# Kernel optimization log

Hardware: AMD Instinct MI355X
Metric: run time of the kernel (lower is better)

The kernel has to match this reference:

```python
import jax, jax.numpy as jnp
import numpy as np

K = 20
EPS = 1e-5
SLOPE = 0.2


def knn_idx(x, k):
    # x: (B, N, C) -> indices of k nearest neighbors (B, N, k), includes self
    xx = jnp.sum(x * x, axis=-1)                       # (B, N)
    inner = jnp.einsum('bnc,bmc->bnm', x, x)           # (B, N, N)
    neg_d = 2.0 * inner - xx[:, :, None] - xx[:, None, :]  # -||xi-xj||^2
    return jax.lax.top_k(neg_d, k)[1]                  # (B, N, k)


def get_graph_feature(x, k):
    # x: (B, N, C) -> (B, N, k, 2C) = [nbr - center, center]
    idx = knn_idx(x, k)
    nbr = jax.vmap(lambda xb, ib: xb[ib])(x, idx)      # (B, N, k, C) gather
    center = x[:, :, None, :]
    return jnp.concatenate([nbr - center, jnp.broadcast_to(center, nbr.shape)], axis=-1)


def bn(h, axes, g, b):
    # training-mode batch norm over `axes`, channels on last axis
    m = jnp.mean(h, axes, keepdims=True)
    v = jnp.var(h, axes, keepdims=True)
    return (h - m) * jax.lax.rsqrt(v + EPS) * g + b


def leaky(h):
    return jnp.where(h > 0, h, SLOPE * h)


def edge_conv(x, W, g, b):
    # x: (B, N, C) -> (B, N, C_out); 1x1 conv + BN + LeakyReLU + max over k
    f = get_graph_feature(x, K)                        # (B, N, k, 2C)
    h = jnp.einsum('bnkc,oc->bnko', f, W)
    h = leaky(bn(h, (0, 1, 2), g, b))
    return jnp.max(h, axis=2)


def setup_inputs() -> dict:
    key = jax.random.key(0)
    ks = jax.random.split(key, 6)
    B, N = 2, 4096
    x = jax.random.normal(ks[0], (B, 3, N), jnp.float32)

    def w(k_, o, i):
        return jax.random.normal(k_, (o, i), jnp.float32) * (1.0 / np.sqrt(i))

    ones = lambda c: jnp.ones((c,), jnp.float32)
    zeros = lambda c: jnp.zeros((c,), jnp.float32)
    return dict(
        x=x,
        W1=w(ks[1], 64, 6),   g1=ones(64),   b1=zeros(64),
        W2=w(ks[2], 64, 128), g2=ones(64),   b2=zeros(64),
        W3=w(ks[3], 128, 128), g3=ones(128), b3=zeros(128),
        W4=w(ks[4], 256, 256), g4=ones(256), b4=zeros(256),
        W5=w(ks[5], 1024, 512), g5=ones(1024), b5=zeros(1024),
    )


def reference(x, W1, g1, b1, W2, g2, b2, W3, g3, b3, W4, g4, b4, W5, g5, b5):
    xb = x.transpose(0, 2, 1)                          # (B, N, 3)
    x1 = edge_conv(xb, W1, g1, b1)                     # (B, N, 64)
    x2 = edge_conv(x1, W2, g2, b2)                     # (B, N, 64)
    x3 = edge_conv(x2, W3, g3, b3)                     # (B, N, 128)
    x4 = edge_conv(x3, W4, g4, b4)                     # (B, N, 256)
    cat = jnp.concatenate([x1, x2, x3, x4], axis=-1)   # (B, N, 512)
    h = jnp.einsum('bnc,oc->bno', cat, W5)             # (B, N, 1024)
    h = leaky(bn(h, (0, 1), g5, b5))
    return h.transpose(0, 2, 1)                        # (B, 1024, N)
```

## Files before the change

### kernel.cpp

```cpp
#include <hip/hip_runtime.h>
#include <cmath>

#define KNN 20
#define NPTS 4096
#define BATCH 2
#define SLOPE 0.2f
#define BNEPS 1e-5
#define GTK 16
#define MAXCAND 256

typedef unsigned short u16;
typedef __attribute__((ext_vector_type(8))) short bf16x8;
typedef __attribute__((ext_vector_type(4))) float f32x4;
typedef _Float16 h8 __attribute__((ext_vector_type(8)));
typedef _Float16 h4 __attribute__((ext_vector_type(4)));

static __device__ __host__ inline int imin(int a, int b) { return a < b ? a : b; }

__global__ void xtrans_kernel(const float* __restrict__ x, float* __restrict__ xb) {
  int i = blockIdx.x * 256 + threadIdx.x;
  if (i < BATCH * 3 * NPTS) {
    int b = i / (3 * NPTS);
    int r = i - b * 3 * NPTS;
    int c = r / NPTS;
    int n = r - c * NPTS;
    xb[((size_t)b * NPTS + n) * 3 + c] = x[i];
  }
}

__global__ void uprep_kernel(const float* __restrict__ W, float* __restrict__ U, int O, int C) {
  int i = blockIdx.x * 256 + threadIdx.x;
  if (i < C * O) {
    int j = i / O, o = i - j * O;
    float w1 = W[(size_t)o * 2 * C + j];
    float w2 = W[(size_t)o * 2 * C + C + j];
    U[(size_t)j * 2 * O + o] = w1;
    U[(size_t)j * 2 * O + O + o] = w2 - w1;
  }
}

__global__ void xx_kernel(const float* __restrict__ X, int stride, int C, float* __restrict__ xx) {
  int i = blockIdx.x * 256 + threadIdx.x;
  if (i < BATCH * NPTS) {
    const float* r = X + (size_t)i * stride;
    double s = 0.0;
    for (int c = 0; c < C; ++c) s += (double)r[c] * (double)r[c];
    xx[i] = (float)s;
  }
}

__global__ void tobf16_kernel(const float* __restrict__ src, u16* __restrict__ dst, int n4) {
  int i = blockIdx.x * 256 + threadIdx.x;
  if (i < n4) {
    float4 v = *(const float4*)&src[(size_t)i * 4];
    unsigned o[4];
#pragma unroll
    for (int j = 0; j < 4; ++j) {
      unsigned x = __float_as_uint(((const float*)&v)[j]);
      unsigned rr = x + 0x7fff + ((x >> 16) & 1);
      o[j] = rr >> 16;
    }
    uint2 pk;
    pk.x = o[0] | (o[1] << 16);
    pk.y = o[2] | (o[3] << 16);
    *(uint2*)&dst[(size_t)i * 4] = pk;
  }
}

template <bool BT, bool DIST>
__global__ __launch_bounds__(256) void gemm128(const float* __restrict__ A, int lda,
                                               const float* __restrict__ B, int ldb,
                                               void* __restrict__ Cout, int ldc, int K,
                                               const float* __restrict__ xxA,
                                               const float* __restrict__ xxB) {
  __shared__ __align__(16) float sA[GTK][144];
  __shared__ __align__(16) float sB[GTK][144];
  int t = threadIdx.x;
  int tx = t & 15, ty = t >> 4;
  int row0 = blockIdx.y * 128, col0 = blockIdx.x * 128;
  float acc[8][8] = {};

  for (int k0 = 0; k0 < K; k0 += GTK) {
    bool fast = (k0 + GTK <= K);
    if (fast) {
#pragma unroll
      for (int it = 0; it < 2; ++it) {
        int i = t + it * 256;
        int r = i >> 2, q = i & 3;
        const float4 av = *(const float4*)&A[(size_t)(row0 + r) * lda + k0 + q * 4];
        int pr = r + ((r >> 5) << 2);
        sA[q * 4 + 0][pr] = av.x;
        sA[q * 4 + 1][pr] = av.y;
        sA[q * 4 + 2][pr] = av.z;
        sA[q * 4 + 3][pr] = av.w;
      }
    } else {
#pragma unroll
      for (int it = 0; it < 2; ++it) {
        int i = t + it * 256;
        int r = i >> 2, q = i & 3;
        int pr = r + ((r >> 5) << 2);
#pragma unroll
        for (int j = 0; j < 4; ++j) {
          int k = q * 4 + j;
          sA[k][pr] = (k0 + k < K) ? A[(size_t)(row0 + r) * lda + k0 + k] : 0.f;
        }
      }
    }
    if (BT) {
      if (fast) {
#pragma unroll
        for (int it = 0; it < 2; ++it) {
          int i = t + it * 256;
          int r = i >> 2, q = i & 3;
          const float4 bv = *(const float4*)&B[(size_t)(col0 + r) * ldb + k0 + q * 4];
          int pr = r + ((r >> 5) << 2);
          sB[q * 4 + 0][pr] = bv.x;
          sB[q * 4 + 1][pr] = bv.y;
          sB[q * 4 + 2][pr] = bv.z;
          sB[q * 4 + 3][pr] = bv.w;
        }
      } else {
#pragma unroll
        for (int it = 0; it < 2; ++it) {
          int i = t + it * 256;
          int r = i >> 2, q = i & 3;
          int pr = r + ((r >> 5) << 2);
#pragma unroll
          for (int j = 0; j < 4; ++j) {
            int k = q * 4 + j;
            sB[k][pr] = (k0 + k < K) ? B[(size_t)(col0 + r) * ldb + k0 + k] : 0.f;
          }
        }
      }
    } else {
#pragma unroll
      for (int it = 0; it < 2; ++it) {
        int i = t + it * 256;
        int k = i >> 5, nq = (i & 31) * 4;
        int pc = nq + ((nq >> 5) << 2);
        float4 bv = make_float4(0.f, 0.f, 0.f, 0.f);
        if (k0 + k < K) bv = *(const float4*)&B[(size_t)(k0 + k) * ldb + col0 + nq];
        *(float4*)&sB[k][pc] = bv;
      }
    }
    __syncthreads();
    int prA = ty * 8 + ((ty >> 2) << 2);
    int prB = tx * 8 + ((tx >> 2) << 2);
#pragma unroll
    for (int kk = 0; kk < GTK; ++kk) {
      float a[8], b[8];
      *(float4*)&a[0] = *(const float4*)&sA[kk][prA];
      *(float4*)&a[4] = *(const float4*)&sA[kk][prA + 4];
      *(float4*)&b[0] = *(const float4*)&sB[kk][prB];
      *(float4*)&b[4] = *(const float4*)&sB[kk][prB + 4];
#pragma unroll
      for (int i = 0; i < 8; ++i)
#pragma unroll
        for (int j = 0; j < 8; ++j) acc[i][j] += a[i] * b[j];
    }
    __syncthreads();
  }

  if (DIST) {
    _Float16* Ch = (_Float16*)Cout;
#pragma unroll
    for (int i = 0; i < 8; ++i) {
      int gr = row0 + ty * 8 + i;
      float xa = xxA[gr];
      h8 o;
#pragma unroll
      for (int j = 0; j < 8; ++j) {
        int gc = col0 + tx * 8 + j;
        o[j] = (_Float16)(2.f * acc[i][j] - xa - xxB[gc]);
      }
      *(h8*)&Ch[(size_t)gr * ldc + col0 + tx * 8] = o;
    }
  } else {
    float* Cf = (float*)Cout;
#pragma unroll
    for (int i = 0; i < 8; ++i) {
      int gr = row0 + ty * 8 + i;
#pragma unroll
      for (int jq = 0; jq < 2; ++jq) {
        float4 o;
#pragma unroll
        for (int j = 0; j < 4; ++j) ((float*)&o)[j] = acc[i][jq * 4 + j];
        *(float4*)&Cf[(size_t)gr * ldc + col0 + tx * 8 + jq * 4] = o;
      }
    }
  }
}

__global__ __launch_bounds__(256) void gemm_dist_sym_kernel(const float* __restrict__ X, int lda,
                                                            const float* __restrict__ xx,
                                                            _Float16* __restrict__ dist, int K,
                                                            size_t dstride) {
  __shared__ __align__(16) float sA[GTK][144];
  __shared__ __align__(16) float sB[GTK][144];
  int t = threadIdx.x;
  int tx = t & 15, ty = t >> 4;
  const float* Xb = X + (size_t)blockIdx.y * NPTS * lda;
  const float* xxv = xx + (size_t)blockIdx.y * NPTS;
  _Float16* db = dist + (size_t)blockIdx.y * dstride;
  int l = blockIdx.x;
  int bi = (int)((sqrtf(8.f * (float)l + 1.f) - 1.f) * 0.5f);
  while ((bi + 1) * (bi + 2) / 2 <= l) ++bi;
  while (bi * (bi + 1) / 2 > l) --bi;
  int bj = l - bi * (bi + 1) / 2;
  int row0 = bi * 128, col0 = bj * 128;
  float acc[8][8] = {};

  for (int k0 = 0; k0 < K; k0 += GTK) {
#pragma unroll
    for (int it = 0; it < 2; ++it) {
      int i = t + it * 256;
      int r = i >> 2, q = i & 3;
      const float4 av = *(const float4*)&Xb[(size_t)(row0 + r) * lda + k0 + q * 4];
      const float4 bv = *(const float4*)&Xb[(size_t)(col0 + r) * lda + k0 + q * 4];
      int pr = r + ((r >> 5) << 2);
      sA[q * 4 + 0][pr] = av.x;
      sA[q * 4 + 1][pr] = av.y;
      sA[q * 4 + 2][pr] = av.z;
      sA[q * 4 + 3][pr] = av.w;
      sB[q * 4 + 0][pr] = bv.x;
      sB[q * 4 + 1][pr] = bv.y;
      sB[q * 4 + 2][pr] = bv.z;
      sB[q * 4 + 3][pr] = bv.w;
    }
    __syncthreads();
    int prA = ty * 8 + ((ty >> 2) << 2);
    int prB = tx * 8 + ((tx >> 2) << 2);
#pragma unroll
    for (int kk = 0; kk < GTK; ++kk) {
      float a[8], b[8];
      *(float4*)&a[0] = *(const float4*)&sA[kk][prA];
      *(float4*)&a[4] = *(const float4*)&sA[kk][prA + 4];
      *(float4*)&b[0] = *(const float4*)&sB[kk][prB];
      *(float4*)&b[4] = *(const float4*)&sB[kk][prB + 4];
#pragma unroll
      for (int i = 0; i < 8; ++i)
#pragma unroll
        for (int j = 0; j < 8; ++j) acc[i][j] += a[i] * b[j];
    }
    __syncthreads();
  }

  {
    float xa[8], xb_[8];
#pragma unroll
    for (int i = 0; i < 8; ++i) xa[i] = xxv[row0 + ty * 8 + i];
#pragma unroll
    for (int j = 0; j < 8; ++j) xb_[j] = xxv[col0 + tx * 8 + j];
#pragma unroll
    for (int i = 0; i < 8; ++i)
#pragma unroll
      for (int j = 0; j < 8; ++j) acc[i][j] = 2.f * acc[i][j] - xa[i] - xb_[j];
  }
#pragma unroll
  for (int i = 0; i < 8; ++i) {
    h8 o;
#pragma unroll
    for (int j = 0; j < 8; ++j) o[j] = (_Float16)acc[i][j];
    *(h8*)&db[(size_t)(row0 + ty * 8 + i) * NPTS + col0 + tx * 8] = o;
  }
  if (bi != bj) {
#pragma unroll
    for (int j = 0; j < 8; ++j) {
      h8 o;
#pragma unroll
      for (int i = 0; i < 8; ++i) o[i] = (_Float16)acc[i][j];
      *(h8*)&db[(size_t)(col0 + tx * 8 + j) * NPTS + row0 + ty * 8] = o;
    }
  }
}

__global__ __launch_bounds__(256) void fc_mfma_kernel(const u16* __restrict__ A,
                                                      const u16* __restrict__ B,
                                                      float* __restrict__ C) {
  __shared__ u16 sA[128][56];
  __shared__ u16 sB[128][56];
  int t = threadIdx.x;
  int lane = t & 63, wave = t >> 6;
  int row0 = blockIdx.y * 128, col0 = blockIdx.x * 128;
  int wr = (wave >> 1) * 64, wc = (wave & 1) * 64;
  int m = lane & 15, q = lane >> 4;
  f32x4 acc[4][4];
#pragma unroll
  for (int i = 0; i < 4; ++i)
#pragma unroll
    for (int j = 0; j < 4; ++j) acc[i][j] = (f32x4){0.f, 0.f, 0.f, 0.f};
  for (int k0 = 0; k0 < 512; k0 += 32) {
#pragma unroll
    for (int it = 0; it < 2; ++it) {
      int i = t + it * 256;
      int r = i >> 2, ch = (i & 3) * 8;
      *(uint4*)&sA[r][ch] = *(const uint4*)&A[(size_t)(row0 + r) * 512 + k0 + ch];
      *(uint4*)&sB[r][ch] = *(const uint4*)&B[(size_t)(col0 + r) * 512 + k0 + ch];
    }
    __syncthreads();
    bf16x8 af[4], bf[4];
#pragma unroll
    for (int i = 0; i < 4; ++i) af[i] = *(const bf16x8*)&sA[wr + i * 16 + m][q * 8];
#pragma unroll
    for (int j = 0; j < 4; ++j) bf[j] = *(const bf16x8*)&sB[wc + j * 16 + m][q * 8];
#pragma unroll
    for (int i = 0; i < 4; ++i)
#pragma unroll
      for (int j = 0; j < 4; ++j)
        acc[i][j] = __builtin_amdgcn_mfma_f32_16x16x32_bf16(af[i], bf[j], acc[i][j], 0, 0, 0);
    __syncthreads();
  }
#pragma unroll
  for (int i = 0; i < 4; ++i)
#pragma unroll
    for (int j = 0; j < 4; ++j)
#pragma unroll
      for (int reg = 0; reg < 4; ++reg)
        C[(size_t)(row0 + wr + i * 16 + q * 4 + reg) * 1024 + col0 + wc + j * 16 + m] =
            acc[i][j][reg];
}

__device__ inline bool comp_less(double v, int i, double ov, int oi) {
  return (v < ov) || (v == ov && i > oi);
}

__global__ __launch_bounds__(256) void topk_fast_kernel(const _Float16* __restrict__ dist,
                                                        size_t dstride,
                                                        const float* __restrict__ Xb,
                                                        size_t xstride, int lda, int C,
                                                        int* __restrict__ idxout, size_t istride,
                                                        int n0, int rows) {
  __shared__ int scand[4][MAXCAND];
  int wave = threadIdx.x >> 6, lane = threadIdx.x & 63;
  int row = blockIdx.x * 4 + wave;
  if (row >= rows) return;
  const _Float16* distb = dist + (size_t)blockIdx.y * dstride;
  const float* Xbb = Xb + (size_t)blockIdx.y * xstride;
  int* idxb = idxout + (size_t)blockIdx.y * istride;
  const _Float16* d = distb + (size_t)row * NPTS;
  float v[16][4];
  float lmax = -__builtin_inff();
#pragma unroll
  for (int s = 0; s < 16; ++s) {
    h4 hv = *(const h4*)&d[s * 256 + lane * 4];
#pragma unroll
    for (int c = 0; c < 4; ++c) {
      v[s][c] = (float)hv[c];
      lmax = fmaxf(lmax, v[s][c]);
    }
  }

  float sv = lmax;
  for (int k = 2; k <= 64; k <<= 1) {
    for (int j = k >> 1; j > 0; j >>= 1) {
      float ov = __shfl_xor(sv, j);
      bool up = ((lane & k) == 0);
      bool lower = ((lane & j) == 0);
      bool mineLess = sv < ov;
      bool keepMine = (up == lower) ? mineLess : !mineLess;
      sv = keepMine ? sv : ov;
    }
  }
  float T = __shfl(sv, 44);

  int myCnt = 0;
#pragma unroll
  for (int s = 0; s < 16; ++s)
#pragma unroll
    for (int c = 0; c < 4; ++c) myCnt += (v[s][c] >= T) ? 1 : 0;
  int ofs = myCnt;
  for (int dlt = 1; dlt < 64; dlt <<= 1) {
    int o = __shfl_up(ofs, dlt);
    if (lane >= dlt) ofs += o;
  }
  int total = __shfl(ofs, 63);
  ofs -= myCnt;
  int w = ofs;
#pragma unroll
  for (int s = 0; s < 16; ++s)
#pragma unroll
    for (int c = 0; c < 4; ++c) {
      if (v[s][c] >= T) {
        if (w < MAXCAND) scand[wave][w] = s * 256 + lane * 4 + c;
        ++w;
      }
    }
  int cnt = imin(total, MAXCAND);
  int gn = n0 + row;
  const float* crow = Xbb + (size_t)gn * lda;
  int nch = (cnt + 63) >> 6;

  double runV = -__builtin_inf();
  int runI = 0x7fffffff;
  for (int ch = 0; ch < nch; ++ch) {
    int slot = ch * 64 + lane;
    int m = (slot < cnt) ? scand[wave][slot] : -1;
    double val = -__builtin_inf();
    int vi = 0x7fffffff;
    if (m >= 0) {
      const float* mrow = Xbb + (size_t)m * lda;
      double dd = 0.0;
      for (int c = 0; c < C; c += 4) {
        float4 a = *(const float4*)&crow[c];
        float4 b = *(const float4*)&mrow[c];
#pragma unroll
        for (int qq = 0; qq < 4; ++qq) {
          double df = (double)((const float*)&a)[qq] - (double)((const float*)&b)[qq];
          dd = fma(df, df, dd);
        }
      }
      val = -dd;
      vi = m;
    }
    for (int k = 2; k <= 64; k <<= 1) {
      for (int j = k >> 1; j > 0; j >>= 1) {
        double ov = __shfl_xor(val, j);
        int oi = __shfl_xor(vi, j);
        bool up = ((lane & k) == 0);
        bool lower = ((lane & j) == 0);
        bool mineLess = comp_less(val, vi, ov, oi);
        bool keepMine = (up == lower) ? mineLess : !mineLess;
        if (!keepMine) { val = ov; vi = oi; }
      }
    }
    if (ch == 0) {
      runV = val;
      runI = vi;
    } else {
      double rv = __shfl(val, 63 - lane);
      int ri = __shfl(vi, 63 - lane);
      if (comp_less(runV, runI, rv, ri)) { runV = rv; runI = ri; }
      for (int j = 32; j > 0; j >>= 1) {
        double ov = __shfl_xor(runV, j);
        int oi = __shfl_xor(runI, j);
        bool lower = ((lane & j) == 0);
        bool mineLess = comp_less(runV, runI, ov, oi);
        bool keepMine = lower ? mineLess : !mineLess;
        if (!keepMine) { runV = ov; runI = oi; }
      }
    }
  }
  if (lane >= 44) idxb[(size_t)gn * KNN + (63 - lane)] = runI;
}

__global__ __launch_bounds__(256) void dist3_topk_kernel(const float* __restrict__ Xb,
                                                         int* __restrict__ idxout) {
  __shared__ float xs[NPTS], ys[NPTS], zs[NPTS];
  __shared__ int scand[4][MAXCAND];
  int t = threadIdx.x;
  const float* Xbb = Xb + (size_t)blockIdx.y * NPTS * 3;
  for (int i = t; i < NPTS * 3; i += 256) {
    int n = i / 3, c = i - n * 3;
    float v = Xbb[i];
    if (c == 0) xs[n] = v;
    else if (c == 1) ys[n] = v;
    else zs[n] = v;
  }
  __syncthreads();
  int wave = t >> 6, lane = t & 63;
  int row = blockIdx.x * 4 + wave;
  float cx = xs[row], cy = ys[row], cz = zs[row];
  float v[16][4];
  float lmax = -__builtin_inff();
#pragma unroll
  for (int s = 0; s < 16; ++s)
#pragma unroll
    for (int c = 0; c < 4; ++c) {
      int m = s * 256 + c * 64 + lane;
      float dx = cx - xs[m], dy = cy - ys[m], dz = cz - zs[m];
      float dv = -(dx * dx + dy * dy + dz * dz);
      v[s][c] = dv;
      lmax = fmaxf(lmax, dv);
    }

  float sv = lmax;
  for (int k = 2; k <= 64; k <<= 1) {
    for (int j = k >> 1; j > 0; j >>= 1) {
      float ov = __shfl_xor(sv, j);
      bool up = ((lane & k) == 0);
      bool lower = ((lane & j) == 0);
      bool mineLess = sv < ov;
      bool keepMine = (up == lower) ? mineLess : !mineLess;
      sv = keepMine ? sv : ov;
    }
  }
  float T = __shfl(sv, 44);

  int myCnt = 0;
#pragma unroll
  for (int s = 0; s < 16; ++s)
#pragma unroll
    for (int c = 0; c < 4; ++c) myCnt += (v[s][c] >= T) ? 1 : 0;
  int ofs = myCnt;
  for (int dlt = 1; dlt < 64; dlt <<= 1) {
    int o = __shfl_up(ofs, dlt);
    if (lane >= dlt) ofs += o;
  }
  int total = __shfl(ofs, 63);
  ofs -= myCnt;
  int w = ofs;
#pragma unroll
  for (int s = 0; s < 16; ++s)
#pragma unroll
    for (int c = 0; c < 4; ++c) {
      if (v[s][c] >= T) {
        if (w < MAXCAND) scand[wave][w] = s * 256 + c * 64 + lane;
        ++w;
      }
    }
  int cnt = imin(total, MAXCAND);
  int nch = (cnt + 63) >> 6;

  double runV = -__builtin_inf();
  int runI = 0x7fffffff;
  for (int ch = 0; ch < nch; ++ch) {
    int slot = ch * 64 + lane;
    int m = (slot < cnt) ? scand[wave][slot] : -1;
    double val = -__builtin_inf();
    int vi = 0x7fffffff;
    if (m >= 0) {
      double dx = (double)cx - (double)xs[m];
      double dy = (double)cy - (double)ys[m];
      double dz = (double)cz - (double)zs[m];
      val = -(dx * dx + dy * dy + dz * dz);
      vi = m;
    }
    for (int k = 2; k <= 64; k <<= 1) {
      for (int j = k >> 1; j > 0; j >>= 1) {
        double ov = __shfl_xor(val, j);
        int oi = __shfl_xor(vi, j);
        bool up = ((lane & k) == 0);
        bool lower = ((lane & j) == 0);
        bool mineLess = comp_less(val, vi, ov, oi);
        bool keepMine = (up == lower) ? mineLess : !mineLess;
        if (!keepMine) { val = ov; vi = oi; }
      }
    }
    if (ch == 0) {
      runV = val;
      runI = vi;
    } else {
      double rv = __shfl(val, 63 - lane);
      int ri = __shfl(vi, 63 - lane);
      if (comp_less(runV, runI, rv, ri)) { runV = rv; runI = ri; }
      for (int j = 32; j > 0; j >>= 1) {
        double ov = __shfl_xor(runV, j);
        int oi = __shfl_xor(runI, j);
        bool lower = ((lane & j) == 0);
        bool mineLess = comp_less(runV, runI, ov, oi);
        bool keepMine = lower ? mineLess : !mineLess;
        if (!keepMine) { runV = ov; runI = oi; }
      }
    }
  }
  if (lane >= 44)
    idxout[((size_t)blockIdx.y * NPTS + row) * KNN + (63 - lane)] = runI;
}

template <int NO>
__global__ __launch_bounds__(256) void gathermax_kernel(const float* __restrict__ PQ,
                                                        const int* __restrict__ idx,
                                                        float* __restrict__ hmax, int O,
                                                        double* __restrict__ pbuf) {
  __shared__ double sh1[4][256];
  __shared__ double sh2[4][256];
  int t = threadIdx.x;
  int wave = t >> 6, lane = t & 63;
  int pt = blockIdx.x * 4 + wave;
  int b = pt >> 12;
  int O2 = 2 * O;
  int iv = idx[(size_t)pt * KNN + (lane % KNN)];
  const float* Qp = PQ + (size_t)pt * O2 + O + lane * NO;
  float q[NO], mx[NO];
  double s1[NO], s2[NO];
#pragma unroll
  for (int c = 0; c < NO; ++c) {
    q[c] = Qp[c];
    mx[c] = -__builtin_inff();
    s1[c] = 0.0;
    s2[c] = 0.0;
  }
#pragma unroll
  for (int k = 0; k < KNN; ++k) {
    int m = __shfl(iv, k);
    const float* Pp = PQ + ((size_t)(b << 12) + m) * O2 + lane * NO;
    float p[NO];
#pragma unroll
    for (int c = 0; c < NO; ++c) p[c] = Pp[c];
#pragma unroll
    for (int c = 0; c < NO; ++c) {
      float h = p[c] + q[c];
      mx[c] = fmaxf(mx[c], h);
      double hd = (double)h;
      s1[c] += hd;
      s2[c] += hd * hd;
    }
  }
  float* Hp = hmax + (size_t)pt * O + lane * NO;
#pragma unroll
  for (int c = 0; c < NO; ++c) {
    Hp[c] = mx[c];
    sh1[wave][lane * NO + c] = s1[c];
    sh2[wave][lane * NO + c] = s2[c];
  }
  __syncthreads();
  if (t < O) {
    double a = 0.0, bb = 0.0;
#pragma unroll
    for (int w = 0; w < 4; ++w) {
      a += sh1[w][t];
      bb += sh2[w][t];
    }
    pbuf[(size_t)blockIdx.x * O2 + t] = a;
    pbuf[(size_t)blockIdx.x * O2 + O + t] = bb;
  }
}

__global__ __launch_bounds__(256) void bn_reduce_finalize(const double* __restrict__ pbuf,
                                                          int nblk, int O,
                                                          const float* __restrict__ g,
                                                          const float* __restrict__ bb,
                                                          double invcount,
                                                          float* __restrict__ s_out,
                                                          float* __restrict__ t_out) {
  __shared__ double sh1[256];
  __shared__ double sh2[256];
  int o = blockIdx.x;
  int t = threadIdx.x;
  double s1 = 0.0, s2 = 0.0;
  for (int blk = t; blk < nblk; blk += 256) {
    s1 += pbuf[(size_t)blk * 2 * O + o];
    s2 += pbuf[(size_t)blk * 2 * O + O + o];
  }
  sh1[t] = s1;
  sh2[t] = s2;
  __syncthreads();
  for (int s = 128; s > 0; s >>= 1) {
    if (t < s) {
      sh1[t] += sh1[t + s];
      sh2[t] += sh2[t + s];
    }
    __syncthreads();
  }
  if (t == 0) {
    double mean = sh1[0] * invcount;
    double var = sh2[0] * invcount - mean * mean;
    double s = (double)g[o] / sqrt(var + BNEPS);
    s_out[o] = (float)s;
    t_out[o] = (float)((double)bb[o] - mean * s);
  }
}

__global__ void apply_kernel(const float* __restrict__ hmax, const float* __restrict__ s,
                             const float* __restrict__ tt, float* __restrict__ feat,
                             u16* __restrict__ featbf, int colOff, int logO, int total) {
  int i = blockIdx.x * 256 + threadIdx.x;
  if (i >= total) return;
  int O = 1 << logO;
  int o = i & (O - 1);
  int pp = i >> logO;
  float v = hmax[i] * s[o] + tt[o];
  float r = v > 0.f ? v : SLOPE * v;
  size_t di = (size_t)pp * 512 + colOff + o;
  feat[di] = r;
  unsigned xbits = __float_as_uint(r);
  unsigned rr = xbits + 0x7fff + ((xbits >> 16) & 1);
  featbf[di] = (u16)(rr >> 16);
}

__global__ void colstats_kernel(const float* __restrict__ H, double* __restrict__ pbuf) {
  int o = blockIdx.x * 256 + threadIdx.x;
  int rb = blockIdx.y;
  int r0 = rb * 128;
  double s1 = 0.0, s2 = 0.0;
  for (int r = 0; r < 128; ++r) {
    double v = (double)H[(size_t)(r0 + r) * 1024 + o];
    s1 += v;
    s2 += v * v;
  }
  pbuf[(size_t)rb * 2048 + o] = s1;
  pbuf[(size_t)rb * 2048 + 1024 + o] = s2;
}

__global__ void out_kernel(const float* __restrict__ h5, const float* __restrict__ s,
                           const float* __restrict__ tt, float* __restrict__ out) {
  __shared__ float tile[32][33];
  int b = blockIdx.z;
  int n0 = blockIdx.x * 32, o0 = blockIdx.y * 32;
  int t = threadIdx.x;
  for (int e = t; e < 1024; e += 256) {
    int rn = e >> 5, co = e & 31;
    int o = o0 + co;
    float v = h5[((size_t)b * NPTS + n0 + rn) * 1024 + o] * s[o] + tt[o];
    tile[rn][co] = v > 0.f ? v : SLOPE * v;
  }
  __syncthreads();
  for (int e = t; e < 1024; e += 256) {
    int ro = e >> 5, cn = e & 31;
    out[((size_t)b * 1024 + o0 + ro) * NPTS + n0 + cn] = tile[cn][ro];
  }
}

extern "C" void kernel_launch(void* const* d_in, const int* in_sizes, int n_in,
                              void* d_out, int out_size, void* d_ws, size_t ws_size,
                              hipStream_t stream) {
  const float* x = (const float*)d_in[0];
  const float* Wm[5] = {(const float*)d_in[1], (const float*)d_in[4], (const float*)d_in[7],
                        (const float*)d_in[10], (const float*)d_in[13]};
  const float* gv[5] = {(const float*)d_in[2], (const float*)d_in[5], (const float*)d_in[8],
                        (const float*)d_in[11], (const float*)d_in[14]};
  const float* bvv[5] = {(const float*)d_in[3], (const float*)d_in[6], (const float*)d_in[9],
                         (const float*)d_in[12], (const float*)d_in[15]};
  float* out = (float*)d_out;

  char* wsb = (char*)d_ws;
  size_t off = 0;
  auto alloc = [&](size_t bytes) -> char* {
    off = (off + 255) & ~(size_t)255;
    char* p = wsb + off;
    off += bytes;
    return p;
  };
  float* xb = (float*)alloc((size_t)BATCH * NPTS * 3 * 4);
  float* xxb = (float*)alloc((size_t)BATCH * NPTS * 4);
  int* idxb = (int*)alloc((size_t)BATCH * NPTS * KNN * 4);
  float* feat = (float*)alloc((size_t)BATCH * NPTS * 512 * 4);
  float* hmax = (float*)alloc((size_t)BATCH * NPTS * 256 * 4);
  float* h5 = (float*)alloc((size_t)BATCH * NPTS * 1024 * 4);
  float* PQ = h5;
  float* U1 = (float*)alloc(3 * 128 * 4);
  float* U2 = (float*)alloc(64 * 128 * 4);
  float* U3 = (float*)alloc(64 * 256 * 4);
  float* U4 = (float*)alloc(128 * 512 * 4);
  u16* featbf = (u16*)alloc((size_t)BATCH * NPTS * 512 * 2);
  u16* w5bf = (u16*)alloc((size_t)1024 * 512 * 2);
  double* pbuf = (double*)alloc((size_t)2048 * 512 * 8);
  float* stv = (float*)alloc(3072 * 4);
  off = (off + 255) & ~(size_t)255;
  size_t avail = (ws_size > off) ? (ws_size - off) : 0;
  size_t slab = (size_t)NPTS * NPTS * 2;
  int nbfit = (int)imin((int)(avail / slab), BATCH);
  size_t rmax = avail / ((size_t)NPTS * 2);
  int R;
  if (rmax >= NPTS) R = NPTS;
  else {
    R = (int)(rmax & ~(size_t)127);
    if (R < 128) R = 128;
  }
  _Float16* distbuf = (_Float16*)(wsb + off);

  float* sv[5] = {stv + 0, stv + 128, stv + 256, stv + 512, stv + 1024};
  float* tv[5] = {stv + 64, stv + 192, stv + 384, stv + 768, stv + 2048};
  float* Us[4] = {U1, U2, U3, U4};
  const int Cs[4] = {3, 64, 64, 128};
  const int Osz[4] = {64, 64, 128, 256};
  const int ntile = (NPTS / 128) * (NPTS / 128 + 1) / 2;

  xtrans_kernel<<<(BATCH * 3 * NPTS + 255) / 256, 256, 0, stream>>>(x, xb);
  for (int l = 0; l < 4; ++l)
    uprep_kernel<<<(Cs[l] * Osz[l] + 255) / 256, 256, 0, stream>>>(Wm[l], Us[l], Osz[l], Cs[l]);
  tobf16_kernel<<<(1024 * 512 / 4 + 255) / 256, 256, 0, stream>>>(Wm[4], w5bf, 1024 * 512 / 4);

  auto knn = [&](const float* Xbase, int lda, int C) {
    xx_kernel<<<(BATCH * NPTS + 255) / 256, 256, 0, stream>>>(Xbase, lda, C, xxb);
    size_t selems = (size_t)NPTS * NPTS;
    if (nbfit >= BATCH) {
      gemm_dist_sym_kernel<<<dim3(ntile, BATCH), 256, 0, stream>>>(Xbase, lda, xxb, distbuf, C,
                                                                   selems);
      topk_fast_kernel<<<dim3(NPTS / 4, BATCH), 256, 0, stream>>>(
          distbuf, selems, Xbase, (size_t)NPTS * lda, lda, C, idxb, (size_t)NPTS * KNN, 0, NPTS);
    } else if (nbfit >= 1) {
      for (int b = 0; b < BATCH; ++b) {
        const float* Xb = Xbase + (size_t)b * NPTS * lda;
        gemm_dist_sym_kernel<<<dim3(ntile, 1), 256, 0, stream>>>(Xb, lda, xxb + (size_t)b * NPTS,
                                                                 distbuf, C, 0);
        topk_fast_kernel<<<dim3(NPTS / 4, 1), 256, 0, stream>>>(
            distbuf, 0, Xb, 0, lda, C, idxb + (size_t)b * NPTS * KNN, 0, 0, NPTS);
      }
    } else {
      for (int b = 0; b < BATCH; ++b) {
        const float* Xb = Xbase + (size_t)b * NPTS * lda;
        for (int n0 = 0; n0 < NPTS; n0 += R) {
          int rows = imin(R, NPTS - n0);
          gemm128<true, true><<<dim3(NPTS / 128, rows / 128), 256, 0, stream>>>(
              Xb + (size_t)n0 * lda, lda, Xb, lda, (void*)distbuf, NPTS, C,
              xxb + (size_t)b * NPTS + n0, xxb + (size_t)b * NPTS);
          topk_fast_kernel<<<dim3(rows / 4, 1), 256, 0, stream>>>(
              distbuf, 0, Xb, 0, lda, C, idxb + (size_t)b * NPTS * KNN, 0, n0, rows);
        }
      }
    }
  };

  auto edge = [&](int li, const float* Xbase, int lda, int C, int O, int colOff) {
    if (li == 0) {
      dist3_topk_kernel<<<dim3(NPTS / 4, BATCH), 256, 0, stream>>>(Xbase, idxb);
    } else {
      knn(Xbase, lda, C);
    }
    int O2 = 2 * O;
    gemm128<false, false><<<dim3(O2 / 128, BATCH * NPTS / 128), 256, 0, stream>>>(
        Xbase, lda, Us[li], O2, (void*)PQ, O2, C, nullptr, nullptr);
    int nblk = BATCH * NPTS / 4;
    if (O == 64)
      gathermax_kernel<1><<<nblk, 256, 0, stream>>>(PQ, idxb, hmax, O, pbuf);
    else if (O == 128)
      gathermax_kernel<2><<<nblk, 256, 0, stream>>>(PQ, idxb, hmax, O, pbuf);
    else
      gathermax_kernel<4><<<nblk, 256, 0, stream>>>(PQ, idxb, hmax, O, pbuf);
    bn_reduce_finalize<<<O, 256, 0, stream>>>(pbuf, nblk, O, gv[li], bvv[li],
                                              1.0 / ((double)BATCH * NPTS * KNN), sv[li], tv[li]);
    int logO = (O == 64) ? 6 : (O == 128) ? 7 : 8;
    int total = BATCH * NPTS * O;
    apply_kernel<<<(total + 255) / 256, 256, 0, stream>>>(hmax, sv[li], tv[li], feat, featbf,
                                                          colOff, logO, total);
  };

  edge(0, xb, 3, 3, 64, 0);
  edge(1, feat, 512, 64, 64, 64);
  edge(2, feat + 64, 512, 64, 128, 128);
  edge(3, feat + 128, 512, 128, 256, 256);

  fc_mfma_kernel<<<dim3(1024 / 128, BATCH * NPTS / 128), 256, 0, stream>>>(featbf, w5bf, h5);
  colstats_kernel<<<dim3(4, 64), 256, 0, stream>>>(h5, pbuf);
  bn_reduce_finalize<<<1024, 256, 0, stream>>>(pbuf, 64, 1024, gv[4], bvv[4],
                                               1.0 / ((double)BATCH * NPTS), sv[4], tv[4]);
  out_kernel<<<dim3(NPTS / 32, 1024 / 32, BATCH), 256, 0, stream>>>(h5, sv[4], tv[4], out);
}
```

Before: 643.1 us.

## Compute kNN distance tiles with split-bf16 MFMA instead of FP32 FMA

Replaces the FP32 scalar-FMA symmetric distance GEMM with a matrix-core kernel. Point features are first split into high and low bf16 halves by a new kernel. The inner products are then accumulated with three bf16 MFMA products (hi·hi, hi·lo, lo·hi) to keep near-FP32 accuracy. The fp16 output tile is staged through shared memory so both the direct and the transposed stores are coalesced. This costs an extra conversion pass, a split buffer, and a small precision difference that could change neighbour ordering on near-ties.

```diff
diff --git a/kernel.cpp b/kernel.cpp
--- a/kernel.cpp
+++ b/kernel.cpp
@@ -16,6 +16,12 @@
 typedef _Float16 h4 __attribute__((ext_vector_type(4)));
 
 static __device__ __host__ inline int imin(int a, int b) { return a < b ? a : b; }
+
+__device__ inline u16 f2bf(float v) {
+  unsigned x = __float_as_uint(v);
+  unsigned rr = x + 0x7fff + ((x >> 16) & 1);
+  return (u16)(rr >> 16);
+}
 
 __global__ void xtrans_kernel(const float* __restrict__ x, float* __restrict__ xb) {
   int i = blockIdx.x * 256 + threadIdx.x;
@@ -55,16 +61,39 @@
     float4 v = *(const float4*)&src[(size_t)i * 4];
     unsigned o[4];
 #pragma unroll
-    for (int j = 0; j < 4; ++j) {
-      unsigned x = __float_as_uint(((const float*)&v)[j]);
-      unsigned rr = x + 0x7fff + ((x >> 16) & 1);
-      o[j] = rr >> 16;
-    }
+    for (int j = 0; j < 4; ++j) o[j] = f2bf(((const float*)&v)[j]);
     uint2 pk;
     pk.x = o[0] | (o[1] << 16);
     pk.y = o[2] | (o[3] << 16);
     *(uint2*)&dst[(size_t)i * 4] = pk;
   }
+}
+
+__global__ void tosplit_kernel(const float* __restrict__ X, int lda, int C,
+                               u16* __restrict__ hi, u16* __restrict__ lo, int ngroups) {
+  int g = blockIdx.x * 256 + threadIdx.x;
+  if (g >= ngroups) return;
+  int perRow = C >> 2;
+  int r = g / perRow;
+  int cq = (g - r * perRow) * 4;
+  float4 v = *(const float4*)&X[(size_t)r * lda + cq];
+  unsigned ho[4], lo_[4];
+#pragma unroll
+  for (int j = 0; j < 4; ++j) {
+    float f = ((const float*)&v)[j];
+    u16 h = f2bf(f);
+    float hv = __uint_as_float(((unsigned)h) << 16);
+    ho[j] = h;
+    lo_[j] = f2bf(f - hv);
+  }
+  uint2 ph, pl;
+  ph.x = ho[0] | (ho[1] << 16);
+  ph.y = ho[2] | (ho[3] << 16);
+  pl.x = lo_[0] | (lo_[1] << 16);
+  pl.y = lo_[2] | (lo_[3] << 16);
+  size_t di = (size_t)r * C + cq;
+  *(uint2*)&hi[di] = ph;
+  *(uint2*)&lo[di] = pl;
 }
 
 template <bool BT, bool DIST>
@@ -192,15 +221,16 @@
   }
 }
 
-__global__ __launch_bounds__(256) void gemm_dist_sym_kernel(const float* __restrict__ X, int lda,
+__global__ __launch_bounds__(256) void dist_sym_mfma_kernel(const u16* __restrict__ Xhi,
+                                                            const u16* __restrict__ Xlo, int K,
                                                             const float* __restrict__ xx,
-                                                            _Float16* __restrict__ dist, int K,
+                                                            _Float16* __restrict__ dist,
                                                             size_t dstride) {
-  __shared__ __align__(16) float sA[GTK][144];
-  __shared__ __align__(16) float sB[GTK][144];
+  __shared__ __align__(16) u16 smem[20544];
   int t = threadIdx.x;
-  int tx = t & 15, ty = t >> 4;
-  const float* Xb = X + (size_t)blockIdx.y * NPTS * lda;
+  int lane = t & 63, wave = t >> 6;
+  const u16* xh = Xhi + (size_t)blockIdx.y * NPTS * K;
+  const u16* xl = Xlo + (size_t)blockIdx.y * NPTS * K;
   const float* xxv = xx + (size_t)blockIdx.y * NPTS;
   _Float16* db = dist + (size_t)blockIdx.y * dstride;
   int l = blockIdx.x;
@@ -209,68 +239,76 @@
   while (bi * (bi + 1) / 2 > l) --bi;
   int bj = l - bi * (bi + 1) / 2;
   int row0 = bi * 128, col0 = bj * 128;
-  float acc[8][8] = {};
-
-  for (int k0 = 0; k0 < K; k0 += GTK) {
-#pragma unroll
-    for (int it = 0; it < 2; ++it) {
-      int i = t + it * 256;
-      int r = i >> 2, q = i & 3;
-      const float4 av = *(const float4*)&Xb[(size_t)(row0 + r) * lda + k0 + q * 4];
-      const float4 bv = *(const float4*)&Xb[(size_t)(col0 + r) * lda + k0 + q * 4];
-      int pr = r + ((r >> 5) << 2);
-      sA[q * 4 + 0][pr] = av.x;
-      sA[q * 4 + 1][pr] = av.y;
-      sA[q * 4 + 2][pr] = av.z;
-      sA[q * 4 + 3][pr] = av.w;
-      sB[q * 4 + 0][pr] = bv.x;
-      sB[q * 4 + 1][pr] = bv.y;
-      sB[q * 4 + 2][pr] = bv.z;
-      sB[q * 4 + 3][pr] = bv.w;
+  int wr = (wave >> 1) * 64, wc = (wave & 1) * 64;
+  int m = lane & 15, q = lane >> 4;
+  f32x4 acc[4][4];
+#pragma unroll
+  for (int i = 0; i < 4; ++i)
+#pragma unroll
+    for (int j = 0; j < 4; ++j) acc[i][j] = (f32x4){0.f, 0.f, 0.f, 0.f};
+
+  for (int k0 = 0; k0 < K; k0 += 32) {
+#pragma unroll
+    for (int it = 0; it < 8; ++it) {
+      int e = t + it * 256;
+      int a = e >> 9, idx = e & 511;
+      int r = idx >> 2, qq = idx & 3;
+      const u16* src = (a == 0 || a == 2) ? xh : xl;
+      int base = (a < 2) ? row0 : col0;
+      *(uint4*)&smem[a * 5120 + r * 40 + qq * 8] =
+          *(const uint4*)&src[(size_t)(base + r) * K + k0 + qq * 8];
     }
     __syncthreads();
-    int prA = ty * 8 + ((ty >> 2) << 2);
-    int prB = tx * 8 + ((tx >> 2) << 2);
-#pragma unroll
-    for (int kk = 0; kk < GTK; ++kk) {
-      float a[8], b[8];
-      *(float4*)&a[0] = *(const float4*)&sA[kk][prA];
-      *(float4*)&a[4] = *(const float4*)&sA[kk][prA + 4];
-      *(float4*)&b[0] = *(const float4*)&sB[kk][prB];
-      *(float4*)&b[4] = *(const float4*)&sB[kk][prB + 4];
-#pragma unroll
-      for (int i = 0; i < 8; ++i)
-#pragma unroll
-        for (int j = 0; j < 8; ++j) acc[i][j] += a[i] * b[j];
-    }
+    bf16x8 ah[4], al[4], bh[4], bl[4];
+#pragma unroll
+    for (int i = 0; i < 4; ++i) {
+      ah[i] = *(const bf16x8*)&smem[0 * 5120 + (wr + i * 16 + m) * 40 + q * 8];
+      al[i] = *(const bf16x8*)&smem[1 * 5120 + (wr + i * 16 + m) * 40 + q * 8];
+    }
+#pragma unroll
+    for (int j = 0; j < 4; ++j) {
+      bh[j] = *(const bf16x8*)&smem[2 * 5120 + (wc + j * 16 + m) * 40 + q * 8];
+      bl[j] = *(const bf16x8*)&smem[3 * 5120 + (wc + j * 16 + m) * 40 + q * 8];
+    }
+#pragma unroll
+    for (int i = 0; i < 4; ++i)
+#pragma unroll
+      for (int j = 0; j < 4; ++j) {
+        acc[i][j] = __builtin_amdgcn_mfma_f32_16x16x32_bf16(ah[i], bh[j], acc[i][j], 0, 0, 0);
+        acc[i][j] = __builtin_amdgcn_mfma_f32_16x16x32_bf16(ah[i], bl[j], acc[i][j], 0, 0, 0);
+        acc[i][j] = __builtin_amdgcn_mfma_f32_16x16x32_bf16(al[i], bh[j], acc[i][j], 0, 0, 0);
+      }
     __syncthreads();
   }
 
+  _Float16* tile = (_Float16*)smem;
   {
-    float xa[8], xb_[8];
-#pragma unroll
-    for (int i = 0; i < 8; ++i) xa[i] = xxv[row0 + ty * 8 + i];
-#pragma unroll
-    for (int j = 0; j < 8; ++j) xb_[j] = xxv[col0 + tx * 8 + j];
-#pragma unroll
-    for (int i = 0; i < 8; ++i)
-#pragma unroll
-      for (int j = 0; j < 8; ++j) acc[i][j] = 2.f * acc[i][j] - xa[i] - xb_[j];
-  }
-#pragma unroll
-  for (int i = 0; i < 8; ++i) {
-    h8 o;
-#pragma unroll
-    for (int j = 0; j < 8; ++j) o[j] = (_Float16)acc[i][j];
-    *(h8*)&db[(size_t)(row0 + ty * 8 + i) * NPTS + col0 + tx * 8] = o;
+    float xbv[4];
+#pragma unroll
+    for (int j = 0; j < 4; ++j) xbv[j] = xxv[col0 + wc + j * 16 + m];
+#pragma unroll
+    for (int i = 0; i < 4; ++i)
+#pragma unroll
+      for (int reg = 0; reg < 4; ++reg) {
+        int r = wr + i * 16 + q * 4 + reg;
+        float xa = xxv[row0 + r];
+#pragma unroll
+        for (int j = 0; j < 4; ++j)
+          tile[r * 136 + wc + j * 16 + m] = (_Float16)(2.f * acc[i][j][reg] - xa - xbv[j]);
+      }
+  }
+  __syncthreads();
+  for (int e = t; e < 2048; e += 256) {
+    int r = e >> 4, seg = e & 15;
+    *(h8*)&db[(size_t)(row0 + r) * NPTS + col0 + seg * 8] = *(const h8*)&tile[r * 136 + seg * 8];
   }
   if (bi != bj) {
-#pragma unroll
-    for (int j = 0; j < 8; ++j) {
+    for (int e = t; e < 2048; e += 256) {
+      int c = e >> 4, seg = e & 15;
       h8 o;
 #pragma unroll
-      for (int i = 0; i < 8; ++i) o[i] = (_Float16)acc[i][j];
-      *(h8*)&db[(size_t)(col0 + tx * 8 + j) * NPTS + row0 + ty * 8] = o;
+      for (int i = 0; i < 8; ++i) o[i] = tile[(seg * 8 + i) * 136 + c];
+      *(h8*)&db[(size_t)(col0 + c) * NPTS + row0 + seg * 8] = o;
     }
   }
 }
@@ -664,9 +702,7 @@
   float r = v > 0.f ? v : SLOPE * v;
   size_t di = (size_t)pp * 512 + colOff + o;
   feat[di] = r;
-  unsigned xbits = __float_as_uint(r);
-  unsigned rr = xbits + 0x7fff + ((xbits >> 16) & 1);
-  featbf[di] = (u16)(rr >> 16);
+  featbf[di] = f2bf(r);
 }
 
 __global__ void colstats_kernel(const float* __restrict__ H, double* __restrict__ pbuf) {
@@ -735,6 +771,8 @@
   float* U4 = (float*)alloc(128 * 512 * 4);
   u16* featbf = (u16*)alloc((size_t)BATCH * NPTS * 512 * 2);
   u16* w5bf = (u16*)alloc((size_t)1024 * 512 * 2);
+  u16* xhi = (u16*)alloc((size_t)BATCH * NPTS * 128 * 2);
+  u16* xlo = (u16*)alloc((size_t)BATCH * NPTS * 128 * 2);
   double* pbuf = (double*)alloc((size_t)2048 * 512 * 8);
   float* stv = (float*)alloc(3072 * 4);
   off = (off + 255) & ~(size_t)255;
@@ -765,16 +803,21 @@
   auto knn = [&](const float* Xbase, int lda, int C) {
     xx_kernel<<<(BATCH * NPTS + 255) / 256, 256, 0, stream>>>(Xbase, lda, C, xxb);
     size_t selems = (size_t)NPTS * NPTS;
+    if (nbfit >= 1) {
+      int ngroups = BATCH * NPTS * (C / 4);
+      tosplit_kernel<<<(ngroups + 255) / 256, 256, 0, stream>>>(Xbase, lda, C, xhi, xlo, ngroups);
+    }
     if (nbfit >= BATCH) {
-      gemm_dist_sym_kernel<<<dim3(ntile, BATCH), 256, 0, stream>>>(Xbase, lda, xxb, distbuf, C,
+      dist_sym_mfma_kernel<<<dim3(ntile, BATCH), 256, 0, stream>>>(xhi, xlo, C, xxb, distbuf,
                                                                    selems);
       topk_fast_kernel<<<dim3(NPTS / 4, BATCH), 256, 0, stream>>>(
           distbuf, selems, Xbase, (size_t)NPTS * lda, lda, C, idxb, (size_t)NPTS * KNN, 0, NPTS);
     } else if (nbfit >= 1) {
       for (int b = 0; b < BATCH; ++b) {
         const float* Xb = Xbase + (size_t)b * NPTS * lda;
-        gemm_dist_sym_kernel<<<dim3(ntile, 1), 256, 0, stream>>>(Xb, lda, xxb + (size_t)b * NPTS,
-                                                                 distbuf, C, 0);
+        dist_sym_mfma_kernel<<<dim3(ntile, 1), 256, 0, stream>>>(
+            xhi + (size_t)b * NPTS * C, xlo + (size_t)b * NPTS * C, C, xxb + (size_t)b * NPTS,
+            distbuf, 0);
         topk_fast_kernel<<<dim3(NPTS / 4, 1), 256, 0, stream>>>(
             distbuf, 0, Xb, 0, lda, C, idxb + (size_t)b * NPTS * KNN, 0, 0, NPTS);
       }
```

Measured after the change: 602.4 us. -6.3%, faster.
